# Performance work log

Measured on AMD Instinct MI355X. Metric: run time of the kernel, lower is better.

Reference implementation:

```python
import jax, jax.numpy as jnp
import numpy as np

T, B, C, H, W = 4, 8, 256, 16, 16
HEADS = 8
N = H * W
TN = T * N
DH = C // HEADS
DECAY = 0.25

# STE quantizer: fwd round(clamp(x,0,1)); bwd passes grad only where 0<=x<=1
@jax.custom_vjp
def quant1(x):
    return jnp.round(jnp.clip(x, 0.0, 1.0))

def _q_fwd(x):
    return quant1(x), x

def _q_bwd(x, g):
    return (jnp.where((x < 0) | (x > 1), 0.0, g),)

quant1.defvjp(_q_fwd, _q_bwd)

def lif(x):
    # x: [T, ...]; sequential LIF membrane decay + quantize over leading (time) axis
    def step(carry, xt):
        mem_old, spike = carry
        mem = (mem_old - jax.lax.stop_gradient(spike) * 0.5) * DECAY + xt
        s = quant1(mem)
        return (mem, s), s
    z = jnp.zeros_like(x[0])
    _, out = jax.lax.scan(step, (z, z), x)
    return out

def bn1d(x, gamma, beta, mean, var):
    # eval-mode BatchNorm1d over channel axis 1 of [B, Ch, L]
    inv = jax.lax.rsqrt(var + 1e-5)
    return (x - mean[None, :, None]) * (gamma * inv)[None, :, None] + beta[None, :, None]

def _rel_pos_index():
    coords = np.stack(np.meshgrid(np.arange(T), np.arange(H), np.arange(W), indexing='ij'))  # [3,T,H,W]
    cf = coords.reshape(3, -1)                      # [3, TN]
    rc = (cf[:, :, None] - cf[:, None, :]).transpose(1, 2, 0).copy()  # [TN, TN, 3]
    rc[:, :, 0] += T - 1
    rc[:, :, 1] += H - 1
    rc[:, :, 2] += W - 1
    rc[:, :, 0] *= (2 * H - 1) * (2 * W - 1)
    rc[:, :, 1] *= (2 * W - 1)
    return rc.sum(-1)                               # [TN, TN] ints

def _mask():
    m = np.ones((TN, TN), np.float32)
    for t in range(T - 1):
        m[t * N:(t + 1) * N, (t + 1) * N:] = 0.0
    return m

_RPI = jnp.asarray(_rel_pos_index().reshape(-1))
_MASK = jnp.asarray(_mask())


def setup_inputs() -> dict:
    key = jax.random.key(0)
    ks = jax.random.split(key, 13)
    bias_rows = (2 * T - 1) * (2 * H - 1) * (2 * W - 1)
    return {
        'x': jax.random.normal(ks[0], (T, B, C, H, W), jnp.float32),
        'w_qkv': jax.random.normal(ks[1], (3 * C, C), jnp.float32) * 0.05,
        'qkv_gamma': jax.random.uniform(ks[2], (3 * C,), jnp.float32, 0.5, 1.5),
        'qkv_beta': jax.random.normal(ks[3], (3 * C,), jnp.float32) * 0.1,
        'qkv_mean': jax.random.normal(ks[4], (3 * C,), jnp.float32) * 0.1,
        'qkv_var': jax.random.uniform(ks[5], (3 * C,), jnp.float32, 0.5, 1.5),
        'bias_table': jax.random.normal(ks[6], (bias_rows, HEADS), jnp.float32) * 0.02,
        'w_proj': jax.random.normal(ks[7], (C, C), jnp.float32) * 0.05,
        'b_proj': jax.random.normal(ks[8], (C,), jnp.float32) * 0.02,
        'proj_gamma': jax.random.uniform(ks[9], (C,), jnp.float32, 0.5, 1.5),
        'proj_beta': jax.random.normal(ks[10], (C,), jnp.float32) * 0.1,
        'proj_mean': jax.random.normal(ks[11], (C,), jnp.float32) * 0.1,
        'proj_var': jax.random.uniform(ks[12], (C,), jnp.float32, 0.5, 1.5),
    }


def reference(x, w_qkv, qkv_gamma, qkv_beta, qkv_mean, qkv_var, bias_table,
              w_proj, b_proj, proj_gamma, proj_beta, proj_mean, proj_var):
    # flatten spatial, then raw reshape [T,B,C,N] -> [B,C,T*N] (as in torch source)
    xf = x.reshape(T, B, C, N).reshape(B, C, T * N)
    # 1x1 conv == channel matmul, then eval BN
    qkv = jnp.einsum('oc,bcl->bol', w_qkv, xf)
    qkv = bn1d(qkv, qkv_gamma, qkv_beta, qkv_mean, qkv_var)
    qkv = qkv.reshape(B, 3 * C, T, N).transpose(2, 0, 1, 3)  # [T,B,3C,N]
    qkv = lif(qkv).transpose(1, 0, 3, 2)                      # [B,T,N,3C]
    q, k, v = jnp.split(qkv, 3, axis=-1)                      # each [B,T,N,C]

    def to_heads(z):  # b t n (h d) -> b h (t n) d
        return z.reshape(B, T, N, HEADS, DH).transpose(0, 3, 1, 2, 4).reshape(B, HEADS, TN, DH)
    q, k, v = map(to_heads, (q, k, v))

    bias = bias_table[_RPI].reshape(TN, TN, HEADS).transpose(2, 0, 1)  # [h,TN,TN]
    attn = jnp.einsum('bhnd,bhmd->bhnm', q, k) + bias[None]
    attn = attn * _MASK[None, None]                                     # block upper-triangle mask
    o = jnp.einsum('bhnm,bhmd->bhnd', attn, v) * 0.125                  # [B,h,TN,d]

    o = o.transpose(0, 2, 1, 3).reshape(B, TN, C).reshape(B, T, N, C).transpose(1, 0, 3, 2)  # [T,B,C,N]
    o = lif(o)
    o = o.transpose(1, 2, 0, 3).reshape(B, C, T * N)          # [B,C,TN]
    o = jnp.einsum('oc,bcl->bol', w_proj, o) + b_proj[None, :, None]
    o = bn1d(o, proj_gamma, proj_beta, proj_mean, proj_var)
    o = o.reshape(B, C, T, N).transpose(2, 0, 1, 3).reshape(T, B, C, H, W)
    return lif(o)
```

## Files before the change

kernel.cpp:

```cpp
#include <hip/hip_runtime.h>
#include <stdint.h>
#include <math.h>

constexpr int T_ = 4;
constexpr int B_ = 8;
constexpr int C_ = 256;
constexpr int N_ = 256;
constexpr int TN_ = 1024;
constexpr int NH_ = 8;
constexpr int O3_ = 768;
constexpr int BIAS_ROWS_ = 6727;

__device__ __constant__ int TI_OF[10] = {0,1,1,2,2,2,3,3,3,3};
__device__ __constant__ int TJ_OF[10] = {0,0,1,0,1,2,0,1,2,3};

__device__ __forceinline__ float quant1f(float m) {
    return rintf(fminf(fmaxf(m, 0.0f), 1.0f));
}

__global__ __launch_bounds__(256, 1) void k1_qkv_gemm(
    const float* __restrict__ x, const float* __restrict__ w,
    const float* __restrict__ gamma, const float* __restrict__ beta,
    const float* __restrict__ mean, const float* __restrict__ var,
    float* __restrict__ out)
{
    __shared__ float At[16][100];
    __shared__ float Bt[16][264];
    const int b = blockIdx.z;
    const int oBase = blockIdx.y * 96;
    const int lBase = blockIdx.x * 256;
    const int tid = threadIdx.x;
    const int tx = tid & 31;
    const int ty = tid >> 5;
    const float* xb = x + (size_t)b * C_ * TN_;

    float acc[12][8];
#pragma unroll
    for (int i = 0; i < 12; ++i)
#pragma unroll
        for (int j = 0; j < 8; ++j) acc[i][j] = 0.0f;

    const int a_row = tid >> 3, a_k2 = (tid & 7) * 2;
    const int b_kk = tid >> 4, b_c16 = (tid & 15) * 16;

    for (int kc = 0; kc < 16; ++kc) {
        const int k0 = kc * 16;
#pragma unroll
        for (int r = 0; r < 3; ++r) {
            const int row = a_row + 32 * r;
            const float2 v = *(const float2*)&w[(size_t)(oBase + row) * C_ + k0 + a_k2];
            At[a_k2][row] = v.x;
            At[a_k2 + 1][row] = v.y;
        }
#pragma unroll
        for (int r = 0; r < 4; ++r) {
            const float4 v = *(const float4*)&xb[(size_t)(k0 + b_kk) * TN_ + lBase + b_c16 + 4 * r];
            *(float4*)&Bt[b_kk][b_c16 + 4 * r] = v;
        }
        __syncthreads();
#pragma unroll
        for (int cc = 0; cc < 16; ++cc) {
            float a[12], bb[8];
            *(float4*)&a[0] = *(const float4*)&At[cc][ty * 4];
            *(float4*)&a[4] = *(const float4*)&At[cc][32 + ty * 4];
            *(float4*)&a[8] = *(const float4*)&At[cc][64 + ty * 4];
            *(float4*)&bb[0] = *(const float4*)&Bt[cc][tx * 8];
            *(float4*)&bb[4] = *(const float4*)&Bt[cc][tx * 8 + 4];
#pragma unroll
            for (int i = 0; i < 12; ++i)
#pragma unroll
                for (int j = 0; j < 8; ++j) acc[i][j] += a[i] * bb[j];
        }
        __syncthreads();
    }

#pragma unroll
    for (int i = 0; i < 12; ++i) {
        const int o = oBase + (i >> 2) * 32 + ty * 4 + (i & 3);
        const float inv = 1.0f / sqrtf(var[o] + 1e-5f);
        const float g = gamma[o] * inv;
        const float mn = mean[o], bt = beta[o];
        float4 s0, s1;
        s0.x = (acc[i][0] - mn) * g + bt;
        s0.y = (acc[i][1] - mn) * g + bt;
        s0.z = (acc[i][2] - mn) * g + bt;
        s0.w = (acc[i][3] - mn) * g + bt;
        s1.x = (acc[i][4] - mn) * g + bt;
        s1.y = (acc[i][5] - mn) * g + bt;
        s1.z = (acc[i][6] - mn) * g + bt;
        s1.w = (acc[i][7] - mn) * g + bt;
        float* dst = &out[((size_t)b * O3_ + o) * TN_ + lBase + tx * 8];
        *(float4*)&dst[0] = s0;
        *(float4*)&dst[4] = s1;
    }
}

__global__ __launch_bounds__(256) void k2_lif_pack(
    const float* __restrict__ qkv,
    uint32_t* __restrict__ qb, uint32_t* __restrict__ kb, uint32_t* __restrict__ vb)
{
    const int tid = threadIdx.x;
    const int g = blockIdx.x;
    const int b = blockIdx.y;
    const int n = blockIdx.z * 128 + (tid >> 1);
    const int dh = tid & 1;
    const int dbase = dh * 16;
    const int which = g >> 3, h = g & 7;
    uint32_t* dst = (which == 0) ? qb : (which == 1) ? kb : vb;
    const float* src = qkv + ((size_t)b * O3_ + g * 32 + dbase) * TN_;

    float memv[16];
#pragma unroll
    for (int d = 0; d < 16; ++d) memv[d] = 0.0f;
    uint32_t prevFull = 0;

    for (int t = 0; t < T_; ++t) {
        uint32_t bits = 0;
#pragma unroll
        for (int dd = 0; dd < 16; ++dd) {
            const float xv = src[(size_t)dd * TN_ + t * N_ + n];
            const float m = (memv[dd] - 0.5f * (float)((prevFull >> (dbase + dd)) & 1u)) * 0.25f + xv;
            memv[dd] = m;
            const float s = quant1f(m);
            bits |= ((uint32_t)s) << (dbase + dd);
        }
        const uint32_t full = bits | (uint32_t)__shfl_xor((int)bits, 1);
        prevFull = full;
        if (dh == 0)
            dst[((size_t)b * NH_ + h) * TN_ + t * N_ + n] = full;
    }
}

__global__ __launch_bounds__(256) void k3_tg(
    const uint32_t* __restrict__ kb, const uint32_t* __restrict__ vb,
    float* __restrict__ Gf)
{
    __shared__ uint64_t ks[4][32][4];
    __shared__ uint64_t vs[4][32][4];
    const int bh = blockIdx.x;
    const int tid = threadIdx.x;
    const int q = tid >> 6, lane = tid & 63;

#pragma unroll
    for (int t = 0; t < T_; ++t) {
        const int j = t * N_ + q * 64 + lane;
        const uint32_t kw = kb[(size_t)bh * TN_ + j];
        const uint32_t vw = vb[(size_t)bh * TN_ + j];
#pragma unroll
        for (int d = 0; d < 32; ++d) {
            const uint64_t mk = __ballot((kw >> d) & 1u);
            const uint64_t mv = __ballot((vw >> d) & 1u);
            if (lane == 0) { ks[t][d][q] = mk; vs[t][d][q] = mv; }
        }
    }
    __syncthreads();

    const int d = tid & 31;
#pragma unroll
    for (int s = 0; s < 4; ++s) {
        const int d2 = (tid >> 5) + 8 * s;
        int cum = 0;
#pragma unroll
        for (int t = 0; t < T_; ++t) {
            int p = 0;
#pragma unroll
            for (int w = 0; w < 4; ++w) p += __popcll(ks[t][d2][w] & vs[t][d][w]);
            cum += p;
            Gf[(size_t)(bh * 4 + t) * 1024 + d2 * 32 + d] = (float)cum;
        }
    }
}

__global__ __launch_bounds__(256) void k3_s1(
    const uint32_t* __restrict__ qb, const float* __restrict__ Gf,
    float* __restrict__ oatt)
{
    const int grp = blockIdx.x;
    const int ti = grp >> 2, seg = grp & 3;
    const int h = blockIdx.y;
    const int b = blockIdx.z;
    const int bh = b * NH_ + h;
    const int tid = threadIdx.x;
    const int d = tid & 31;
    const int ig = tid >> 5;

    const float* gsrc = Gf + (size_t)(bh * 4 + ti) * 1024 + d;
    float g[32];
#pragma unroll
    for (int d2 = 0; d2 < 32; ++d2) g[d2] = gsrc[d2 * 32];

    const uint32_t* qbh = qb + (size_t)bh * TN_;
    const int i0 = ti * N_ + seg * 64 + ig * 8;
#pragma unroll
    for (int s = 0; s < 8; ++s) {
        const int i = i0 + s;
        const uint32_t q = qbh[i];
        float acc = 0.0f;
#pragma unroll
        for (int d2 = 0; d2 < 32; ++d2)
            acc += ((q >> d2) & 1u) ? g[d2] : 0.0f;
        oatt[((size_t)b * TN_ + i) * C_ + h * 32 + d] = acc;
    }
}

__global__ __launch_bounds__(256) void k3_bias_gemm(
    const uint32_t* __restrict__ vb, const float* __restrict__ bias_table,
    float* __restrict__ p0, float* __restrict__ p1,
    float* __restrict__ p2, float* __restrict__ p3)
{
    __shared__ float sbl[640];
    __shared__ float At[16][68];
    __shared__ float Bt[16][132];

    const int z = blockIdx.z;
    const int h = z / 10;
    const int p = z % 10;
    const int ti = TI_OF[p], tj = TJ_OF[p];
    const int dt = ti - tj;
    const int iT = blockIdx.y;
    const int nBase = blockIdx.x * 128;
    const int tid = threadIdx.x;

    const int base = 3363 + 961 * dt + 124 * iT - 480;
    for (int s = tid; s < 640; s += 256) {
        const int gidx = base + s;
        sbl[s] = (gidx < BIAS_ROWS_) ? bias_table[(size_t)gidx * NH_ + h] : 0.0f;
    }

    const int ty = tid >> 4, tx = tid & 15;

    const int ccS = tx;
    const int iBase4 = ty * 4;
    const int sIdxBase = 31 * (iBase4 >> 4) + (iBase4 & 15) + 480 - ccS;

    const int kkS = ty;
    const int n8 = tx * 8;
    const int nS = nBase + n8;
    const int bS = nS >> 5, d0S = nS & 31;
    const uint32_t* vbw = vb + ((size_t)bS * NH_ + h) * TN_ + tj * 256 + kkS;

    float acc[4][8];
#pragma unroll
    for (int i = 0; i < 4; ++i)
#pragma unroll
        for (int j = 0; j < 8; ++j) acc[i][j] = 0.0f;

    __syncthreads();

    for (int kc = 0; kc < 16; ++kc) {
        {
            const int s0 = sIdxBase - 31 * kc;
            float4 av;
            av.x = sbl[s0];
            av.y = sbl[s0 + 1];
            av.z = sbl[s0 + 2];
            av.w = sbl[s0 + 3];
            *(float4*)&At[ccS][iBase4] = av;
        }
        {
            const uint32_t wd = vbw[kc * 16];
            float4 b0, b1;
            b0.x = (float)((wd >> d0S) & 1u);
            b0.y = (float)((wd >> (d0S + 1)) & 1u);
            b0.z = (float)((wd >> (d0S + 2)) & 1u);
            b0.w = (float)((wd >> (d0S + 3)) & 1u);
            b1.x = (float)((wd >> (d0S + 4)) & 1u);
            b1.y = (float)((wd >> (d0S + 5)) & 1u);
            b1.z = (float)((wd >> (d0S + 6)) & 1u);
            b1.w = (float)((wd >> (d0S + 7)) & 1u);
            *(float4*)&Bt[kkS][n8] = b0;
            *(float4*)&Bt[kkS][n8 + 4] = b1;
        }
        __syncthreads();
#pragma unroll
        for (int cc = 0; cc < 16; ++cc) {
            float a[4], bb[8];
            *(float4*)&a[0] = *(const float4*)&At[cc][ty * 4];
            *(float4*)&bb[0] = *(const float4*)&Bt[cc][tx * 8];
            *(float4*)&bb[4] = *(const float4*)&Bt[cc][tx * 8 + 4];
#pragma unroll
            for (int i = 0; i < 4; ++i)
#pragma unroll
                for (int j = 0; j < 8; ++j) acc[i][j] += a[i] * bb[j];
        }
        __syncthreads();
    }

    float* plane = (tj == 0) ? p0 : (tj == 1) ? p1 : (tj == 2) ? p2 : p3;
    const int nrows = (4 - tj) * 256;
    const int c0 = h * 32 + d0S;
#pragma unroll
    for (int r = 0; r < 4; ++r) {
        const int rowL = dt * 256 + iT * 64 + ty * 4 + r;
        float* dst = &plane[((size_t)bS * nrows + rowL) * 256 + c0];
        float4 s0, s1;
        s0.x = acc[r][0]; s0.y = acc[r][1]; s0.z = acc[r][2]; s0.w = acc[r][3];
        s1.x = acc[r][4]; s1.y = acc[r][5]; s1.z = acc[r][6]; s1.w = acc[r][7];
        *(float4*)&dst[0] = s0;
        *(float4*)&dst[4] = s1;
    }
}

__global__ __launch_bounds__(256) void k4_lif2(
    const float* __restrict__ oatt,
    const float* __restrict__ p0, const float* __restrict__ p1,
    const float* __restrict__ p2, const float* __restrict__ p3,
    uint32_t* __restrict__ s2c)
{
    const int c = threadIdx.x;
    const int n = blockIdx.x;
    const int b = blockIdx.y;
    const int lane = c & 63;
    float memv = 0.0f, spk = 0.0f;
    for (int t = 0; t < T_; ++t) {
        const int l = t * N_ + n;
        float v = oatt[((size_t)b * TN_ + l) * C_ + c];
        v += p0[((size_t)b * 1024 + l) * 256 + c];
        if (t >= 1) v += p1[((size_t)b * 768 + (l - 256)) * 256 + c];
        if (t >= 2) v += p2[((size_t)b * 512 + (l - 512)) * 256 + c];
        if (t >= 3) v += p3[((size_t)b * 256 + (l - 768)) * 256 + c];
        const float m = (memv - 0.5f * spk) * 0.25f + 0.125f * v;
        memv = m;
        const float s = quant1f(m);
        spk = s;
        const uint64_t mask = __ballot(s != 0.0f);
        if (lane == 0)
            s2c[((size_t)b * TN_ + l) * 8 + (c >> 5)] = (uint32_t)mask;
        else if (lane == 32)
            s2c[((size_t)b * TN_ + l) * 8 + (c >> 5)] = (uint32_t)(mask >> 32);
    }
}

__global__ __launch_bounds__(256) void k5_proj_lif(
    const uint32_t* __restrict__ s2c, const float* __restrict__ w,
    const float* __restrict__ bp,
    const float* __restrict__ gamma, const float* __restrict__ beta,
    const float* __restrict__ mean, const float* __restrict__ var,
    float* __restrict__ out)
{
    __shared__ float At[128][36];
    __shared__ uint32_t Sw[128 * 9];
    const int nBase = blockIdx.x * 32;
    const int oBase = blockIdx.y * 32;
    const int b = blockIdx.z;
    const int tid = threadIdx.x;
    const int tx = tid & 31;
    const int ty = tid >> 5;

#pragma unroll
    for (int j = 0; j < 4; ++j) {
        const int fidx = tid * 4 + j;
        const int lp = fidx >> 3, wsel = fidx & 7;
        const int t = lp >> 5, nn = lp & 31;
        Sw[lp * 9 + wsel] = s2c[((size_t)b * TN_ + t * 256 + nBase + nn) * 8 + wsel];
    }

    const int a_row = tid >> 3, a_kq = (tid & 7) * 16;

    float acc[4][4];
#pragma unroll
    for (int r = 0; r < 4; ++r)
#pragma unroll
        for (int t = 0; t < 4; ++t) acc[r][t] = 0.0f;

    for (int half = 0; half < 2; ++half) {
        if (half) __syncthreads();
#pragma unroll
        for (int j = 0; j < 4; ++j) {
            const float4 v = *(const float4*)&w[(size_t)(oBase + a_row) * C_ + half * 128 + a_kq + 4 * j];
            At[a_kq + 4 * j][a_row] = v.x;
            At[a_kq + 4 * j + 1][a_row] = v.y;
            At[a_kq + 4 * j + 2][a_row] = v.z;
            At[a_kq + 4 * j + 3][a_row] = v.w;
        }
        __syncthreads();

        for (int ks = 0; ks < 4; ++ks) {
            uint32_t wr[4];
#pragma unroll
            for (int t = 0; t < 4; ++t)
                wr[t] = Sw[(t * 32 + tx) * 9 + half * 4 + ks];
#pragma unroll
            for (int u = 0; u < 32; ++u) {
                float a[4];
                *(float4*)&a[0] = *(const float4*)&At[ks * 32 + u][ty * 4];
                float bv[4];
#pragma unroll
                for (int t = 0; t < 4; ++t) bv[t] = (float)((wr[t] >> u) & 1u);
#pragma unroll
                for (int r = 0; r < 4; ++r)
#pragma unroll
                    for (int t = 0; t < 4; ++t) acc[r][t] += a[r] * bv[t];
            }
        }
    }

#pragma unroll
    for (int r = 0; r < 4; ++r) {
        const int o = oBase + ty * 4 + r;
        const float inv = 1.0f / sqrtf(var[o] + 1e-5f);
        const float g = gamma[o] * inv;
        const float mn = mean[o], bt = beta[o], bpo = bp[o];
        float memv = 0.0f, spk = 0.0f;
#pragma unroll
        for (int t = 0; t < 4; ++t) {
            const float val = ((acc[r][t] + bpo) - mn) * g + bt;
            const float m = (memv - 0.5f * spk) * 0.25f + val;
            memv = m;
            const float s = quant1f(m);
            spk = s;
            out[(((size_t)t * B_ + b) * C_ + o) * N_ + nBase + tx] = s;
        }
    }
}

extern "C" void kernel_launch(void* const* d_in, const int* in_sizes, int n_in,
                              void* d_out, int out_size, void* d_ws, size_t ws_size,
                              hipStream_t stream)
{
    const float* x          = (const float*)d_in[0];
    const float* w_qkv      = (const float*)d_in[1];
    const float* qkv_gamma  = (const float*)d_in[2];
    const float* qkv_beta   = (const float*)d_in[3];
    const float* qkv_mean   = (const float*)d_in[4];
    const float* qkv_var    = (const float*)d_in[5];
    const float* bias_table = (const float*)d_in[6];
    const float* w_proj     = (const float*)d_in[7];
    const float* b_proj     = (const float*)d_in[8];
    const float* proj_gamma = (const float*)d_in[9];
    const float* proj_beta  = (const float*)d_in[10];
    const float* proj_mean  = (const float*)d_in[11];
    const float* proj_var   = (const float*)d_in[12];
    float* out = (float*)d_out;

    char* ws = (char*)d_ws;
    float*    qkv_bn = (float*)(ws + 0);
    float*    Gf     = (float*)(ws + 524288);
    float*    part0  = (float*)(ws + 1048576);
    float*    part1  = (float*)(ws + 9437184);
    float*    part2  = (float*)(ws + 15728640);
    float*    part3  = (float*)(ws + 19922944);
    float*    oatt   = (float*)(ws + 25165824);
    uint32_t* s2c    = (uint32_t*)(ws + 33554432);
    uint32_t* qbits  = (uint32_t*)(ws + 50331648);
    uint32_t* kbits  = (uint32_t*)(ws + 50593792);
    uint32_t* vbits  = (uint32_t*)(ws + 50855936);

    k1_qkv_gemm<<<dim3(4, 8, 8), 256, 0, stream>>>(
        x, w_qkv, qkv_gamma, qkv_beta, qkv_mean, qkv_var, qkv_bn);

    k2_lif_pack<<<dim3(24, 8, 2), 256, 0, stream>>>(qkv_bn, qbits, kbits, vbits);

    k3_tg<<<dim3(64), 256, 0, stream>>>(kbits, vbits, Gf);

    k3_s1<<<dim3(16, 8, 8), 256, 0, stream>>>(qbits, Gf, oatt);

    k3_bias_gemm<<<dim3(2, 4, 80), 256, 0, stream>>>(
        vbits, bias_table, part0, part1, part2, part3);

    k4_lif2<<<dim3(256, 8), 256, 0, stream>>>(oatt, part0, part1, part2, part3, s2c);

    k5_proj_lif<<<dim3(8, 8, 8), 256, 0, stream>>>(
        s2c, w_proj, b_proj, proj_gamma, proj_beta, proj_mean, proj_var, out);
}
```

Measured before the change: 250.9 us.

## Fuse q·G attention product into LIF kernel and retile QKV GEMM

```diff
diff --git a/kernel.cpp b/kernel.cpp
--- a/kernel.cpp
+++ b/kernel.cpp
@@ -18,80 +18,72 @@
     return rintf(fminf(fmaxf(m, 0.0f), 1.0f));
 }
 
-__global__ __launch_bounds__(256, 1) void k1_qkv_gemm(
+__global__ __launch_bounds__(256) void k1_qkv_gemm(
     const float* __restrict__ x, const float* __restrict__ w,
     const float* __restrict__ gamma, const float* __restrict__ beta,
     const float* __restrict__ mean, const float* __restrict__ var,
     float* __restrict__ out)
 {
-    __shared__ float At[16][100];
-    __shared__ float Bt[16][264];
+    __shared__ float At[16][68];
+    __shared__ float Bt[16][132];
     const int b = blockIdx.z;
-    const int oBase = blockIdx.y * 96;
-    const int lBase = blockIdx.x * 256;
+    const int oBase = blockIdx.y * 64;
+    const int lBase = blockIdx.x * 128;
     const int tid = threadIdx.x;
     const int tx = tid & 31;
     const int ty = tid >> 5;
     const float* xb = x + (size_t)b * C_ * TN_;
 
-    float acc[12][8];
-#pragma unroll
-    for (int i = 0; i < 12; ++i)
-#pragma unroll
-        for (int j = 0; j < 8; ++j) acc[i][j] = 0.0f;
-
+    float acc[8][4];
+#pragma unroll
+    for (int i = 0; i < 8; ++i)
+#pragma unroll
+        for (int j = 0; j < 4; ++j) acc[i][j] = 0.0f;
+
+    const int b_kk = tid >> 4, b_c4 = (tid & 15) * 4;
     const int a_row = tid >> 3, a_k2 = (tid & 7) * 2;
-    const int b_kk = tid >> 4, b_c16 = (tid & 15) * 16;
 
     for (int kc = 0; kc < 16; ++kc) {
         const int k0 = kc * 16;
 #pragma unroll
-        for (int r = 0; r < 3; ++r) {
+        for (int r = 0; r < 2; ++r) {
             const int row = a_row + 32 * r;
             const float2 v = *(const float2*)&w[(size_t)(oBase + row) * C_ + k0 + a_k2];
             At[a_k2][row] = v.x;
             At[a_k2 + 1][row] = v.y;
         }
 #pragma unroll
-        for (int r = 0; r < 4; ++r) {
-            const float4 v = *(const float4*)&xb[(size_t)(k0 + b_kk) * TN_ + lBase + b_c16 + 4 * r];
-            *(float4*)&Bt[b_kk][b_c16 + 4 * r] = v;
+        for (int r = 0; r < 2; ++r) {
+            const float4 v = *(const float4*)&xb[(size_t)(k0 + b_kk) * TN_ + lBase + b_c4 + 64 * r];
+            *(float4*)&Bt[b_kk][b_c4 + 64 * r] = v;
         }
         __syncthreads();
 #pragma unroll
         for (int cc = 0; cc < 16; ++cc) {
-            float a[12], bb[8];
+            float a[8], bb[4];
             *(float4*)&a[0] = *(const float4*)&At[cc][ty * 4];
             *(float4*)&a[4] = *(const float4*)&At[cc][32 + ty * 4];
-            *(float4*)&a[8] = *(const float4*)&At[cc][64 + ty * 4];
-            *(float4*)&bb[0] = *(const float4*)&Bt[cc][tx * 8];
-            *(float4*)&bb[4] = *(const float4*)&Bt[cc][tx * 8 + 4];
-#pragma unroll
-            for (int i = 0; i < 12; ++i)
-#pragma unroll
-                for (int j = 0; j < 8; ++j) acc[i][j] += a[i] * bb[j];
+            *(float4*)&bb[0] = *(const float4*)&Bt[cc][tx * 4];
+#pragma unroll
+            for (int i = 0; i < 8; ++i)
+#pragma unroll
+                for (int j = 0; j < 4; ++j) acc[i][j] += a[i] * bb[j];
         }
         __syncthreads();
     }
 
 #pragma unroll
-    for (int i = 0; i < 12; ++i) {
+    for (int i = 0; i < 8; ++i) {
         const int o = oBase + (i >> 2) * 32 + ty * 4 + (i & 3);
         const float inv = 1.0f / sqrtf(var[o] + 1e-5f);
         const float g = gamma[o] * inv;
         const float mn = mean[o], bt = beta[o];
-        float4 s0, s1;
-        s0.x = (acc[i][0] - mn) * g + bt;
-        s0.y = (acc[i][1] - mn) * g + bt;
-        s0.z = (acc[i][2] - mn) * g + bt;
-        s0.w = (acc[i][3] - mn) * g + bt;
-        s1.x = (acc[i][4] - mn) * g + bt;
-        s1.y = (acc[i][5] - mn) * g + bt;
-        s1.z = (acc[i][6] - mn) * g + bt;
-        s1.w = (acc[i][7] - mn) * g + bt;
-        float* dst = &out[((size_t)b * O3_ + o) * TN_ + lBase + tx * 8];
-        *(float4*)&dst[0] = s0;
-        *(float4*)&dst[4] = s1;
+        float4 st;
+        st.x = (acc[i][0] - mn) * g + bt;
+        st.y = (acc[i][1] - mn) * g + bt;
+        st.z = (acc[i][2] - mn) * g + bt;
+        st.w = (acc[i][3] - mn) * g + bt;
+        *(float4*)&out[((size_t)b * O3_ + o) * TN_ + lBase + tx * 4] = st;
     }
 }
 
@@ -99,35 +91,30 @@
     const float* __restrict__ qkv,
     uint32_t* __restrict__ qb, uint32_t* __restrict__ kb, uint32_t* __restrict__ vb)
 {
-    const int tid = threadIdx.x;
+    const int n = threadIdx.x;
     const int g = blockIdx.x;
     const int b = blockIdx.y;
-    const int n = blockIdx.z * 128 + (tid >> 1);
-    const int dh = tid & 1;
-    const int dbase = dh * 16;
     const int which = g >> 3, h = g & 7;
     uint32_t* dst = (which == 0) ? qb : (which == 1) ? kb : vb;
-    const float* src = qkv + ((size_t)b * O3_ + g * 32 + dbase) * TN_;
-
-    float memv[16];
-#pragma unroll
-    for (int d = 0; d < 16; ++d) memv[d] = 0.0f;
-    uint32_t prevFull = 0;
+    const float* src = qkv + ((size_t)b * O3_ + g * 32) * TN_;
+
+    float memv[32];
+#pragma unroll
+    for (int d = 0; d < 32; ++d) memv[d] = 0.0f;
+    uint32_t prev = 0;
 
     for (int t = 0; t < T_; ++t) {
         uint32_t bits = 0;
 #pragma unroll
-        for (int dd = 0; dd < 16; ++dd) {
-            const float xv = src[(size_t)dd * TN_ + t * N_ + n];
-            const float m = (memv[dd] - 0.5f * (float)((prevFull >> (dbase + dd)) & 1u)) * 0.25f + xv;
-            memv[dd] = m;
+        for (int d = 0; d < 32; ++d) {
+            const float xv = src[(size_t)d * TN_ + t * N_ + n];
+            const float m = (memv[d] - 0.5f * (float)((prev >> d) & 1u)) * 0.25f + xv;
+            memv[d] = m;
             const float s = quant1f(m);
-            bits |= ((uint32_t)s) << (dbase + dd);
-        }
-        const uint32_t full = bits | (uint32_t)__shfl_xor((int)bits, 1);
-        prevFull = full;
-        if (dh == 0)
-            dst[((size_t)b * NH_ + h) * TN_ + t * N_ + n] = full;
+            bits |= ((uint32_t)s) << d;
+        }
+        prev = bits;
+        dst[((size_t)b * NH_ + h) * TN_ + t * N_ + n] = bits;
     }
 }
 
@@ -168,38 +155,6 @@
             cum += p;
             Gf[(size_t)(bh * 4 + t) * 1024 + d2 * 32 + d] = (float)cum;
         }
-    }
-}
-
-__global__ __launch_bounds__(256) void k3_s1(
-    const uint32_t* __restrict__ qb, const float* __restrict__ Gf,
-    float* __restrict__ oatt)
-{
-    const int grp = blockIdx.x;
-    const int ti = grp >> 2, seg = grp & 3;
-    const int h = blockIdx.y;
-    const int b = blockIdx.z;
-    const int bh = b * NH_ + h;
-    const int tid = threadIdx.x;
-    const int d = tid & 31;
-    const int ig = tid >> 5;
-
-    const float* gsrc = Gf + (size_t)(bh * 4 + ti) * 1024 + d;
-    float g[32];
-#pragma unroll
-    for (int d2 = 0; d2 < 32; ++d2) g[d2] = gsrc[d2 * 32];
-
-    const uint32_t* qbh = qb + (size_t)bh * TN_;
-    const int i0 = ti * N_ + seg * 64 + ig * 8;
-#pragma unroll
-    for (int s = 0; s < 8; ++s) {
-        const int i = i0 + s;
-        const uint32_t q = qbh[i];
-        float acc = 0.0f;
-#pragma unroll
-        for (int d2 = 0; d2 < 32; ++d2)
-            acc += ((q >> d2) & 1u) ? g[d2] : 0.0f;
-        oatt[((size_t)b * TN_ + i) * C_ + h * 32 + d] = acc;
     }
 }
 
@@ -302,7 +257,7 @@
 }
 
 __global__ __launch_bounds__(256) void k4_lif2(
-    const float* __restrict__ oatt,
+    const uint32_t* __restrict__ qb, const float* __restrict__ Gf,
     const float* __restrict__ p0, const float* __restrict__ p1,
     const float* __restrict__ p2, const float* __restrict__ p3,
     uint32_t* __restrict__ s2c)
@@ -311,10 +266,19 @@
     const int n = blockIdx.x;
     const int b = blockIdx.y;
     const int lane = c & 63;
+    const int h = c >> 5, d = c & 31;
+    const int bh = b * NH_ + h;
+    const uint32_t* qbh = qb + (size_t)bh * TN_;
+
     float memv = 0.0f, spk = 0.0f;
     for (int t = 0; t < T_; ++t) {
         const int l = t * N_ + n;
-        float v = oatt[((size_t)b * TN_ + l) * C_ + c];
+        const uint32_t q = qbh[l];
+        const float* g = Gf + (size_t)(bh * 4 + t) * 1024 + d;
+        float v = 0.0f;
+#pragma unroll
+        for (int d2 = 0; d2 < 32; ++d2)
+            v += ((q >> d2) & 1u) ? g[d2 * 32] : 0.0f;
         v += p0[((size_t)b * 1024 + l) * 256 + c];
         if (t >= 1) v += p1[((size_t)b * 768 + (l - 256)) * 256 + c];
         if (t >= 2) v += p2[((size_t)b * 512 + (l - 512)) * 256 + c];
@@ -435,30 +399,28 @@
 
     char* ws = (char*)d_ws;
     float*    qkv_bn = (float*)(ws + 0);
-    float*    Gf     = (float*)(ws + 524288);
     float*    part0  = (float*)(ws + 1048576);
     float*    part1  = (float*)(ws + 9437184);
     float*    part2  = (float*)(ws + 15728640);
     float*    part3  = (float*)(ws + 19922944);
-    float*    oatt   = (float*)(ws + 25165824);
+    float*    Gf     = (float*)(ws + 25165824);
     uint32_t* s2c    = (uint32_t*)(ws + 33554432);
     uint32_t* qbits  = (uint32_t*)(ws + 50331648);
     uint32_t* kbits  = (uint32_t*)(ws + 50593792);
     uint32_t* vbits  = (uint32_t*)(ws + 50855936);
 
-    k1_qkv_gemm<<<dim3(4, 8, 8), 256, 0, stream>>>(
+    k1_qkv_gemm<<<dim3(8, 12, 8), 256, 0, stream>>>(
         x, w_qkv, qkv_gamma, qkv_beta, qkv_mean, qkv_var, qkv_bn);
 
-    k2_lif_pack<<<dim3(24, 8, 2), 256, 0, stream>>>(qkv_bn, qbits, kbits, vbits);
+    k2_lif_pack<<<dim3(24, 8), 256, 0, stream>>>(qkv_bn, qbits, kbits, vbits);
 
     k3_tg<<<dim3(64), 256, 0, stream>>>(kbits, vbits, Gf);
-
-    k3_s1<<<dim3(16, 8, 8), 256, 0, stream>>>(qbits, Gf, oatt);
 
     k3_bias_gemm<<<dim3(2, 4, 80), 256, 0, stream>>>(
         vbits, bias_table, part0, part1, part2, part3);
 
-    k4_lif2<<<dim3(256, 8), 256, 0, stream>>>(oatt, part0, part1, part2, part3, s2c);
+    k4_lif2<<<dim3(256, 8), 256, 0, stream>>>(
+        qbits, Gf, part0, part1, part2, part3, s2c);
 
     k5_proj_lif<<<dim3(8, 8, 8), 256, 0, stream>>>(
         s2c, w_proj, b_proj, proj_gamma, proj_beta, proj_mean, proj_var, out);
```

After: 231.6 us. 1.08x faster.
